# Kernel tuning notes

Measured on AMD Instinct MI355X. Metric: run time of the kernel, lower is better.

## Reference

```python
import jax, jax.numpy as jnp
import numpy as np

N, C = 262144, 128

def setup_inputs() -> dict:
    key = jax.random.key(0)
    k1, k2 = jax.random.split(key)
    x = jax.random.normal(k1, (N, C), dtype=jnp.float32)
    # binary label matrix (0/1 floats), as implied by the _target[i][0]==0 check
    target = jax.random.randint(k2, (N, C), 0, 2).astype(jnp.float32)
    return {"x": x, "target": target}

def reference(x, target):
    # Per-row argmax over classes (torch.max(_input[i], 0) -> idx)
    idx = jnp.argmax(x, axis=1)                      # [N]
    # Rows where idx > 0 and target[i,0] == 0 get all non-idx target entries zeroed
    cond = (idx > 0) & (target[:, 0] == 0)           # [N]
    keep = jax.nn.one_hot(idx, x.shape[1], dtype=target.dtype)  # [N, C]
    t = jnp.where(cond[:, None], target * keep, target)
    return jnp.mean(jnp.abs(x * t))
```

## Files before the change

### kernel.cpp

```cpp
#include <hip/hip_runtime.h>

#define NROWS 262144
#define NCOLS 128
#define NBLOCKS 4096
#define TPB 256
#define WAVES_PER_BLOCK (TPB / 64)

__global__ __launch_bounds__(TPB) void biased_loss_partial(
    const float* __restrict__ x, const float* __restrict__ t,
    float* __restrict__ partial)
{
    const int lane = threadIdx.x & 63;
    const int waveInBlock = threadIdx.x >> 6;
    const int globalWave = blockIdx.x * WAVES_PER_BLOCK + waveInBlock;
    const int totalWaves = gridDim.x * WAVES_PER_BLOCK;

    const int half = lane >> 5;
    const int sub  = lane & 31;

    float acc = 0.0f;

    const int npairs = NROWS / 2;
    for (int p = globalWave; p < npairs; p += totalWaves) {
        const int row = p * 2 + half;
        const size_t base = (size_t)row * NCOLS + (size_t)sub * 4;
        const float4 xv = *(const float4*)(x + base);
        const float4 tv = *(const float4*)(t + base);

        int c = sub * 4;
        float bv = xv.x; int bi = c;
        if (xv.y > bv) { bv = xv.y; bi = c + 1; }
        if (xv.z > bv) { bv = xv.z; bi = c + 2; }
        if (xv.w > bv) { bv = xv.w; bi = c + 3; }

        #pragma unroll
        for (int off = 16; off > 0; off >>= 1) {
            float ov = __shfl_xor(bv, off, 64);
            int   oi = __shfl_xor(bi, off, 64);
            if (ov > bv || (ov == bv && oi < bi)) { bv = ov; bi = oi; }
        }

        float t0 = __shfl(tv.x, half << 5, 64);
        const bool cond = (bi > 0) && (t0 == 0.0f);

        float c0 = fabsf(xv.x * tv.x);
        float c1 = fabsf(xv.y * tv.y);
        float c2 = fabsf(xv.z * tv.z);
        float c3 = fabsf(xv.w * tv.w);

        float s;
        if (cond) {
            s = (c     == bi ? c0 : 0.0f)
              + (c + 1 == bi ? c1 : 0.0f)
              + (c + 2 == bi ? c2 : 0.0f)
              + (c + 3 == bi ? c3 : 0.0f);
        } else {
            s = c0 + c1 + c2 + c3;
        }
        acc += s;
    }

    #pragma unroll
    for (int off = 32; off > 0; off >>= 1)
        acc += __shfl_xor(acc, off, 64);

    __shared__ float smem[WAVES_PER_BLOCK];
    if (lane == 0) smem[waveInBlock] = acc;
    __syncthreads();
    if (threadIdx.x == 0) {
        float b = 0.0f;
        #pragma unroll
        for (int w = 0; w < WAVES_PER_BLOCK; ++w) b += smem[w];
        partial[blockIdx.x] = b;
    }
}

__global__ __launch_bounds__(256) void reduce_partials(
    const float* __restrict__ partial, float* __restrict__ out, int n)
{
    float acc = 0.0f;
    for (int i = threadIdx.x; i < n; i += 256) acc += partial[i];
    #pragma unroll
    for (int off = 32; off > 0; off >>= 1)
        acc += __shfl_xor(acc, off, 64);
    __shared__ float smem[4];
    const int lane = threadIdx.x & 63, w = threadIdx.x >> 6;
    if (lane == 0) smem[w] = acc;
    __syncthreads();
    if (threadIdx.x == 0) {
        float s = smem[0] + smem[1] + smem[2] + smem[3];
        out[0] = s / (float)((size_t)NROWS * (size_t)NCOLS);
    }
}

extern "C" void kernel_launch(void* const* d_in, const int* in_sizes, int n_in,
                              void* d_out, int out_size, void* d_ws, size_t ws_size,
                              hipStream_t stream) {
    const float* x = (const float*)d_in[0];
    const float* t = (const float*)d_in[1];
    float* partial = (float*)d_ws;

    biased_loss_partial<<<NBLOCKS, TPB, 0, stream>>>(x, t, partial);
    reduce_partials<<<1, 256, 0, stream>>>(partial, (float*)d_out, NBLOCKS);
}
```

Before: 281.1 us.

## Process eight rows per wave with 16 elements per lane and fewer shuffles

Each wave now handles eight rows per iteration, with eight lanes per row. Every lane issues four float4 loads each of x and target, so more memory requests are in flight per thread. The per-lane argmax is a register tree reduction that also carries the product value at the argmax, which cuts the cross-lane shuffle reduction from 5 steps to 3. The masked-sum branch is replaced by a select on that carried value, and the grid is halved to 2048 blocks. In exchange, register pressure rises and there are fewer waves to hide latency.

```diff
diff --git a/kernel.cpp b/kernel.cpp
--- a/kernel.cpp
+++ b/kernel.cpp
@@ -2,9 +2,12 @@
 
 #define NROWS 262144
 #define NCOLS 128
-#define NBLOCKS 4096
 #define TPB 256
-#define WAVES_PER_BLOCK (TPB / 64)
+#define WPB (TPB / 64)
+#define NBLOCKS 2048
+#define NWAVES (NBLOCKS * WPB)
+#define ROWS_PER_GROUP 8
+#define NGROUPS (NROWS / ROWS_PER_GROUP)
 
 __global__ __launch_bounds__(TPB) void biased_loss_partial(
     const float* __restrict__ x, const float* __restrict__ t,
@@ -12,65 +15,92 @@
 {
     const int lane = threadIdx.x & 63;
     const int waveInBlock = threadIdx.x >> 6;
-    const int globalWave = blockIdx.x * WAVES_PER_BLOCK + waveInBlock;
-    const int totalWaves = gridDim.x * WAVES_PER_BLOCK;
-
-    const int half = lane >> 5;
-    const int sub  = lane & 31;
+    const int gw = blockIdx.x * WPB + waveInBlock;
+    const int g = lane >> 3;
+    const int s = lane & 7;
 
     float acc = 0.0f;
 
-    const int npairs = NROWS / 2;
-    for (int p = globalWave; p < npairs; p += totalWaves) {
-        const int row = p * 2 + half;
-        const size_t base = (size_t)row * NCOLS + (size_t)sub * 4;
-        const float4 xv = *(const float4*)(x + base);
-        const float4 tv = *(const float4*)(t + base);
+    #pragma unroll 2
+    for (int grp = gw; grp < NGROUPS; grp += NWAVES) {
+        const int row = grp * ROWS_PER_GROUP + g;
+        const float* xr = x + (size_t)row * NCOLS + (size_t)s * 4;
+        const float* tr = t + (size_t)row * NCOLS + (size_t)s * 4;
 
-        int c = sub * 4;
-        float bv = xv.x; int bi = c;
-        if (xv.y > bv) { bv = xv.y; bi = c + 1; }
-        if (xv.z > bv) { bv = xv.z; bi = c + 2; }
-        if (xv.w > bv) { bv = xv.w; bi = c + 3; }
+        float4 xv[4], tv[4];
+        #pragma unroll
+        for (int j = 0; j < 4; ++j) xv[j] = *(const float4*)(xr + j * 32);
+        #pragma unroll
+        for (int j = 0; j < 4; ++j) tv[j] = *(const float4*)(tr + j * 32);
+
+        float xe[16], ce[16];
+        #pragma unroll
+        for (int j = 0; j < 4; ++j) {
+            xe[4*j+0] = xv[j].x; xe[4*j+1] = xv[j].y;
+            xe[4*j+2] = xv[j].z; xe[4*j+3] = xv[j].w;
+            ce[4*j+0] = fabsf(xv[j].x * tv[j].x);
+            ce[4*j+1] = fabsf(xv[j].y * tv[j].y);
+            ce[4*j+2] = fabsf(xv[j].z * tv[j].z);
+            ce[4*j+3] = fabsf(xv[j].w * tv[j].w);
+        }
+
+        float bvv[16]; int bii[16]; float bcc[16];
+        #pragma unroll
+        for (int e = 0; e < 16; ++e) {
+            bvv[e] = xe[e];
+            bii[e] = 32 * (e >> 2) + 4 * s + (e & 3);
+            bcc[e] = ce[e];
+        }
+        #pragma unroll
+        for (int w = 8; w >= 1; w >>= 1) {
+            #pragma unroll
+            for (int e = 0; e < 16; ++e) {
+                if (e < w) {
+                    bool take = bvv[e + w] > bvv[e];
+                    bvv[e] = take ? bvv[e + w] : bvv[e];
+                    bii[e] = take ? bii[e + w] : bii[e];
+                    bcc[e] = take ? bcc[e + w] : bcc[e];
+                }
+            }
+        }
+        float bv = bvv[0]; int bi = bii[0]; float bc = bcc[0];
 
         #pragma unroll
-        for (int off = 16; off > 0; off >>= 1) {
+        for (int off = 4; off > 0; off >>= 1) {
             float ov = __shfl_xor(bv, off, 64);
             int   oi = __shfl_xor(bi, off, 64);
-            if (ov > bv || (ov == bv && oi < bi)) { bv = ov; bi = oi; }
+            float oc = __shfl_xor(bc, off, 64);
+            bool take = (ov > bv) || (ov == bv && oi < bi);
+            bv = take ? ov : bv;
+            bi = take ? oi : bi;
+            bc = take ? oc : bc;
         }
 
-        float t0 = __shfl(tv.x, half << 5, 64);
+        float t0 = __shfl(tv[0].x, g << 3, 64);
         const bool cond = (bi > 0) && (t0 == 0.0f);
 
-        float c0 = fabsf(xv.x * tv.x);
-        float c1 = fabsf(xv.y * tv.y);
-        float c2 = fabsf(xv.z * tv.z);
-        float c3 = fabsf(xv.w * tv.w);
+        #pragma unroll
+        for (int w = 8; w >= 1; w >>= 1) {
+            #pragma unroll
+            for (int e = 0; e < 16; ++e)
+                if (e < w) ce[e] += ce[e + w];
+        }
+        float psum = ce[0];
 
-        float s;
-        if (cond) {
-            s = (c     == bi ? c0 : 0.0f)
-              + (c + 1 == bi ? c1 : 0.0f)
-              + (c + 2 == bi ? c2 : 0.0f)
-              + (c + 3 == bi ? c3 : 0.0f);
-        } else {
-            s = c0 + c1 + c2 + c3;
-        }
-        acc += s;
+        acc += cond ? (s == 0 ? bc : 0.0f) : psum;
     }
 
     #pragma unroll
     for (int off = 32; off > 0; off >>= 1)
         acc += __shfl_xor(acc, off, 64);
 
-    __shared__ float smem[WAVES_PER_BLOCK];
+    __shared__ float smem[WPB];
     if (lane == 0) smem[waveInBlock] = acc;
     __syncthreads();
     if (threadIdx.x == 0) {
         float b = 0.0f;
         #pragma unroll
-        for (int w = 0; w < WAVES_PER_BLOCK; ++w) b += smem[w];
+        for (int w = 0; w < WPB; ++w) b += smem[w];
         partial[blockIdx.x] = b;
     }
 }
```

Result: no change. 279.5 us (-0.5%).

## Assign one row per thread with in-register argmax instead of wave shuffles

Applied to the files above, without the earlier changes.

Switches from two rows per wave, where each lane loads a float4 and a shuffle reduction finds the argmax, to one thread per row. Each thread streams its whole 512-byte row with fully unrolled float4 loads, tracking the argmax and its contribution in registers. This removes the per-row cross-lane shuffles and the grid-stride loop. The cost is uncoalesced access, since adjacent threads read addresses 512 bytes apart, plus higher register pressure from the unrolled loads.

```diff
diff --git a/kernel.cpp b/kernel.cpp
--- a/kernel.cpp
+++ b/kernel.cpp
@@ -1,76 +1,72 @@
 #include <hip/hip_runtime.h>
+#include <math.h>
 
 #define NROWS 262144
 #define NCOLS 128
-#define NBLOCKS 4096
 #define TPB 256
-#define WAVES_PER_BLOCK (TPB / 64)
+#define NBLOCKS (NROWS / TPB)
 
-__global__ __launch_bounds__(TPB) void biased_loss_partial(
+__global__ __launch_bounds__(TPB) void biased_loss_rows(
     const float* __restrict__ x, const float* __restrict__ t,
     float* __restrict__ partial)
 {
-    const int lane = threadIdx.x & 63;
-    const int waveInBlock = threadIdx.x >> 6;
-    const int globalWave = blockIdx.x * WAVES_PER_BLOCK + waveInBlock;
-    const int totalWaves = gridDim.x * WAVES_PER_BLOCK;
+    const int row = blockIdx.x * TPB + threadIdx.x;
+    const float4* xr = (const float4*)(x + (size_t)row * NCOLS);
+    const float4* tr = (const float4*)(t + (size_t)row * NCOLS);
 
-    const int half = lane >> 5;
-    const int sub  = lane & 31;
+    float acc0 = 0.f, acc1 = 0.f;
+    float bv = -INFINITY; int bi = 0; float bc = 0.f;
+    float t0 = 0.f;
 
-    float acc = 0.0f;
+    #pragma unroll
+    for (int j = 0; j < NCOLS / 4; ++j) {
+        const float4 xv = xr[j];
+        const float4 tv = tr[j];
+        if (j == 0) t0 = tv.x;
 
-    const int npairs = NROWS / 2;
-    for (int p = globalWave; p < npairs; p += totalWaves) {
-        const int row = p * 2 + half;
-        const size_t base = (size_t)row * NCOLS + (size_t)sub * 4;
-        const float4 xv = *(const float4*)(x + base);
-        const float4 tv = *(const float4*)(t + base);
+        const float c0 = fabsf(xv.x * tv.x);
+        const float c1 = fabsf(xv.y * tv.y);
+        const float c2 = fabsf(xv.z * tv.z);
+        const float c3 = fabsf(xv.w * tv.w);
+        acc0 += c0 + c1;
+        acc1 += c2 + c3;
 
-        int c = sub * 4;
-        float bv = xv.x; int bi = c;
-        if (xv.y > bv) { bv = xv.y; bi = c + 1; }
-        if (xv.z > bv) { bv = xv.z; bi = c + 2; }
-        if (xv.w > bv) { bv = xv.w; bi = c + 3; }
+        const bool s01 = xv.y > xv.x;
+        const float v01 = s01 ? xv.y : xv.x;
+        const int   i01 = 4 * j + (s01 ? 1 : 0);
+        const float w01 = s01 ? c1 : c0;
 
-        #pragma unroll
-        for (int off = 16; off > 0; off >>= 1) {
-            float ov = __shfl_xor(bv, off, 64);
-            int   oi = __shfl_xor(bi, off, 64);
-            if (ov > bv || (ov == bv && oi < bi)) { bv = ov; bi = oi; }
-        }
+        const bool s23 = xv.w > xv.z;
+        const float v23 = s23 ? xv.w : xv.z;
+        const int   i23 = 4 * j + 2 + (s23 ? 1 : 0);
+        const float w23 = s23 ? c3 : c2;
 
-        float t0 = __shfl(tv.x, half << 5, 64);
-        const bool cond = (bi > 0) && (t0 == 0.0f);
+        const bool sm = v23 > v01;
+        const float vm = sm ? v23 : v01;
+        const int   im = sm ? i23 : i01;
+        const float wm = sm ? w23 : w01;
 
-        float c0 = fabsf(xv.x * tv.x);
-        float c1 = fabsf(xv.y * tv.y);
-        float c2 = fabsf(xv.z * tv.z);
-        float c3 = fabsf(xv.w * tv.w);
+        const bool sb = vm > bv;
+        bv = sb ? vm : bv;
+        bi = sb ? im : bi;
+        bc = sb ? wm : bc;
+    }
 
-        float s;
-        if (cond) {
-            s = (c     == bi ? c0 : 0.0f)
-              + (c + 1 == bi ? c1 : 0.0f)
-              + (c + 2 == bi ? c2 : 0.0f)
-              + (c + 3 == bi ? c3 : 0.0f);
-        } else {
-            s = c0 + c1 + c2 + c3;
-        }
-        acc += s;
-    }
+    const bool cond = (bi > 0) && (t0 == 0.0f);
+    float rowsum = cond ? bc : (acc0 + acc1);
 
     #pragma unroll
     for (int off = 32; off > 0; off >>= 1)
-        acc += __shfl_xor(acc, off, 64);
+        rowsum += __shfl_xor(rowsum, off, 64);
 
-    __shared__ float smem[WAVES_PER_BLOCK];
-    if (lane == 0) smem[waveInBlock] = acc;
+    __shared__ float smem[TPB / 64];
+    const int lane = threadIdx.x & 63, w = threadIdx.x >> 6;
+    if (lane == 0) smem[w] = rowsum;
     __syncthreads();
     if (threadIdx.x == 0) {
-        float b = 0.0f;
+        float b = 0.f;
         #pragma unroll
-        for (int w = 0; w < WAVES_PER_BLOCK; ++w) b += smem[w];
+        for (int i = 0; i < TPB / 64; ++i) b += smem[i];
         partial[blockIdx.x] = b;
     }
 }
@@ -100,6 +96,6 @@
     const float* t = (const float*)d_in[1];
     float* partial = (float*)d_ws;
 
-    biased_loss_partial<<<NBLOCKS, TPB, 0, stream>>>(x, t, partial);
+    biased_loss_rows<<<NBLOCKS, TPB, 0, stream>>>(x, t, partial);
     reduce_partials<<<1, 256, 0, stream>>>(partial, (float*)d_out, NBLOCKS);
 }
```

After: 286.9 us. 1.02x slower.
